# Kernel tuning notes

Hardware: AMD Instinct MI355X
Metric: run time of the kernel (lower is better)

Reference implementation:

```python
import jax, jax.numpy as jnp
import numpy as np

B, L, E, D = 32, 1024, 512, 512  # batch, seq_len, input_size, per-direction hidden
SCALE = 1.4142135623730951  # rescale=True, highway_bias=0 -> sqrt(1+exp(0*2)) = sqrt(2)


def setup_inputs() -> dict:
    key = jax.random.key(0)
    ks = jax.random.split(key, 12)
    g = lambda k, shape, s: (jax.random.normal(k, shape, jnp.float32) * s)
    return {
        "seqs": jax.random.normal(ks[0], (B, L, E), jnp.float32),
        # layer 0: input E -> 2 dirs * 4 projections * D
        "W0": g(ks[1], (E, 8 * D), (1.0 / E) ** 0.5),
        "vf0": g(ks[2], (2, D), 0.1), "vr0": g(ks[3], (2, D), 0.1),
        "bf0": jnp.zeros((2, D), jnp.float32), "br0": jnp.zeros((2, D), jnp.float32),
        # layer 1: input 2D -> 2 dirs * 4 projections * D
        "W1": g(ks[4], (2 * D, 8 * D), (1.0 / (2 * D)) ** 0.5),
        "vf1": g(ks[5], (2, D), 0.1), "vr1": g(ks[6], (2, D), 0.1),
        "bf1": jnp.zeros((2, D), jnp.float32), "br1": jnp.zeros((2, D), jnp.float32),
        "lengths": jax.random.randint(ks[7], (B,), 1, L + 1, dtype=jnp.int32),
    }


def _sru_dir(u, vf, vr, bf, br, reverse):
    # u: (L, B, 4, D) -> h: (L, B, D), c_T: (B, D)
    def step(c, u_t):
        xt, fp, rp, xp = u_t[:, 0], u_t[:, 1], u_t[:, 2], u_t[:, 3]
        f = jax.nn.sigmoid(fp + vf * c + bf)
        c_new = f * c + (1.0 - f) * xt
        r = jax.nn.sigmoid(rp + vr * c + br)
        h = r * c_new + (1.0 - r) * xp * SCALE
        return c_new, h

    c0 = jnp.zeros((u.shape[1], u.shape[-1]), u.dtype)
    cT, hs = jax.lax.scan(step, c0, u, reverse=reverse)
    return hs, cT


def _sru_layer(x, W, vf, vr, bf, br):
    # x: (L, B, n_in)
    Lx, Bx = x.shape[0], x.shape[1]
    U = (x @ W).reshape(Lx, Bx, 2, 4, -1)  # dirs, (x_tilde, f, r, x_resid)
    h_f, c_f = _sru_dir(U[:, :, 0], vf[0], vr[0], bf[0], br[0], False)
    h_b, c_b = _sru_dir(U[:, :, 1], vf[1], vr[1], bf[1], br[1], True)
    return jnp.concatenate([h_f, h_b], -1), jnp.concatenate([c_f, c_b], -1)


def reference(seqs, W0, vf0, vr0, bf0, br0, W1, vf1, vr1, bf1, br1, lengths):
    x = jnp.transpose(seqs, (1, 0, 2))  # (L, B, E)
    out0, _ = _sru_layer(x, W0, vf0, vr0, bf0, br0)
    out1, c1 = _sru_layer(out0, W1, vf1, vr1, bf1, br1)
    # module returns (h[1], output.transpose(0,1)): layer-1 final cell state, (B,L,2D) outputs
    return c1, jnp.transpose(out1, (1, 0, 2))
```

## Files before the change

### kernel.cpp

```cpp
#include <hip/hip_runtime.h>
#include <cstdint>
#include <cstddef>

#define B_   32
#define L_   1024
#define D_   512
#define M_   (B_ * L_)
#define N8D  4096
#define SCALEF 1.4142135623730951f
#define LOG2E 1.4426950408889634f

typedef unsigned short u16;
typedef __bf16 bf16x8 __attribute__((ext_vector_type(8)));
typedef unsigned short u16x8 __attribute__((ext_vector_type(8)));
typedef unsigned short u16x4 __attribute__((ext_vector_type(4)));
typedef float f32x4 __attribute__((ext_vector_type(4)));

__device__ __forceinline__ float bf2f(u16 u) {
    union { unsigned int i; float f; } v; v.i = ((unsigned int)u) << 16; return v.f;
}
__device__ __forceinline__ u16 f2bf(float x) {
    union { float f; unsigned int i; } v; v.f = x;
    unsigned int r = (v.i + 0x7fffu + ((v.i >> 16) & 1u)) >> 16;
    return (u16)r;
}
__device__ __forceinline__ float sigmoid_fast(float z) {
    return __builtin_amdgcn_rcpf(1.0f + __builtin_amdgcn_exp2f(-LOG2E * z));
}

__device__ __forceinline__ void gl2lds16(const u16* g, u16* l) {
    __builtin_amdgcn_global_load_lds(
        (const __attribute__((address_space(1))) void*)g,
        (__attribute__((address_space(3))) void*)l, 16, 0, 0);
}

#define VMW(n) asm volatile("s_waitcnt vmcnt(" #n ")" ::: "memory")

__global__ __launch_bounds__(256) void f32_to_bf16(const float* __restrict__ in,
                                                   u16* __restrict__ out) {
    size_t i = ((size_t)blockIdx.x * 256 + threadIdx.x) * 8;
    f32x4 v0 = *(const f32x4*)(in + i);
    f32x4 v1 = *(const f32x4*)(in + i + 4);
    u16x8 o;
#pragma unroll
    for (int q = 0; q < 4; ++q) { o[q] = f2bf(v0[q]); o[4 + q] = f2bf(v1[q]); }
    *(u16x8*)(out + i) = o;
}

__global__ __launch_bounds__(256) void transpose_w(const float* __restrict__ in,
                                                   u16* __restrict__ out,
                                                   int R, int C) {
    __shared__ u16 tile[32][33];
    int bx = blockIdx.x * 32;
    int by = blockIdx.y * 32;
    int tx = threadIdx.x & 31;
    int ty = threadIdx.x >> 5;
#pragma unroll
    for (int i = 0; i < 32; i += 8)
        tile[ty + i][tx] = f2bf(in[(size_t)(by + ty + i) * C + bx + tx]);
    __syncthreads();
#pragma unroll
    for (int i = 0; i < 32; i += 8) {
        int n = bx + ty + i;
        int p = (n >> 11) * 2048 + ((n & 511) << 2) + ((n >> 9) & 3);
        out[(size_t)p * R + by + tx] = tile[tx][ty + i];
    }
}

__global__ __launch_bounds__(512) void gemm256(const u16* __restrict__ A,
                                               const u16* __restrict__ BT,
                                               u16* __restrict__ U, int K) {
    extern __shared__ __align__(16) u16 lds[];
    const int t    = threadIdx.x;
    const int lane = t & 63;
    const int wave = t >> 6;
    const int wm   = wave >> 2;
    const int wn   = wave & 3;
    const int qm   = lane & 15;
    const int quad = lane >> 4;

    const int nwg = gridDim.x;
    const int wg  = blockIdx.x;
    const int swz = (wg & 7) * (nwg >> 3) + (wg >> 3);
    const int bn  = (swz & 15) << 8;
    const int bm  = (swz >> 4) << 8;

    const int P0   = t * 16;
    const int L0   = P0 ^ ((P0 >> 3) & 0x30);
    const int srow = L0 >> 6;
    const int scol = (L0 & 63) >> 1;
    const u16* Ag = A  + (size_t)(bm + srow) * K + scol;
    const u16* Bg = BT + (size_t)(bn + srow) * K + scol;
    const size_t g128 = (size_t)128 * K;
    u16* ldst = lds + t * 8;

    const int fxor  = (quad * 16) ^ ((qm & 6) << 3);
    const int aBase = (wm * 128 + qm) * 64 + fxor;
    const int bBase = (wn * 64  + qm) * 64 + fxor;
    const char* ldsc = (const char*)lds;

    f32x4 acc[8][4];
#pragma unroll
    for (int i = 0; i < 8; ++i)
#pragma unroll
        for (int j = 0; j < 4; ++j) acc[i][j] = (f32x4)(0.0f);

    bf16x8 bfr[4];

#define STG(op, tile, ks, buf) do {                                          \
        const u16* g_ = ((op) ? Bg : Ag) + (size_t)(tile) * 64 + (ks) * 32;  \
        u16* l_ = ldst + (buf) * 32768 + (op) * 16384 + (ks) * 8192;         \
        gl2lds16(g_, l_);                                                    \
        gl2lds16(g_ + g128, l_ + 4096);                                      \
    } while (0)

#define PHASE(buf, mh, ks, STAGE_STMT, VM_STMT) do {                         \
        const char* As_ = ldsc + ((buf) * 32768 + (ks) * 8192) * 2;          \
        const char* Bs_ = ldsc + ((buf) * 32768 + 16384 + (ks) * 8192) * 2;  \
        bf16x8 a_[4];                                                        \
        _Pragma("unroll")                                                    \
        for (int mi = 0; mi < 4; ++mi)                                       \
            a_[mi] = *(const bf16x8*)(As_ + aBase + ((mh) * 64 + mi * 16) * 64); \
        if ((mh) == 0) {                                                     \
            _Pragma("unroll")                                                \
            for (int nj = 0; nj < 4; ++nj)                                   \
                bfr[nj] = *(const bf16x8*)(Bs_ + bBase + nj * 16 * 64);      \
        }                                                                    \
        STAGE_STMT;                                                          \
        __builtin_amdgcn_s_barrier();                                        \
        asm volatile("s_waitcnt lgkmcnt(0)" ::: "memory");                   \
        __builtin_amdgcn_sched_barrier(0);                                   \
        __builtin_amdgcn_s_setprio(1);                                       \
        _Pragma("unroll")                                                    \
        for (int mi = 0; mi < 4; ++mi)                                       \
            _Pragma("unroll")                                                \
            for (int nj = 0; nj < 4; ++nj)                                   \
                acc[(mh) * 4 + mi][nj] = __builtin_amdgcn_mfma_f32_16x16x32_bf16( \
                    a_[mi], bfr[nj], acc[(mh) * 4 + mi][nj], 0, 0, 0);       \
        __builtin_amdgcn_s_setprio(0);                                       \
        VM_STMT;                                                             \
        __builtin_amdgcn_s_barrier();                                        \
    } while (0)

    const int nt = K >> 6;

    STG(1, 0, 0, 0); STG(0, 0, 0, 0); STG(1, 0, 1, 0); STG(0, 0, 1, 0);
    VMW(4);
    STG(1, 1, 0, 1); STG(0, 1, 0, 1); STG(1, 1, 1, 1);
    VMW(6);
    __builtin_amdgcn_s_barrier();

    const int niter = (nt >> 1) - 1;
    for (int i = 0; i < niter; ++i) {
        const int tp1 = 2 * i + 1, tp2 = 2 * i + 2, tp3 = 2 * i + 3;
        PHASE(0, 0, 0, STG(0, tp1, 1, 1), );
        PHASE(0, 1, 0, STG(1, tp2, 0, 0), );
        PHASE(0, 0, 1, STG(0, tp2, 0, 0), );
        PHASE(0, 1, 1, STG(1, tp2, 1, 0), VMW(6));
        PHASE(1, 0, 0, STG(0, tp2, 1, 0), );
        PHASE(1, 1, 0, STG(1, tp3, 0, 1), );
        PHASE(1, 0, 1, STG(0, tp3, 0, 1), );
        PHASE(1, 1, 1, STG(1, tp3, 1, 1), VMW(6));
    }
    PHASE(0, 0, 0, STG(0, nt - 1, 1, 1), );
    PHASE(0, 1, 0, , );
    PHASE(0, 0, 1, , );
    PHASE(0, 1, 1, , VMW(4));
    PHASE(1, 0, 0, , );
    PHASE(1, 1, 0, , VMW(0));
    PHASE(1, 0, 1, , );
    PHASE(1, 1, 1, , );

#undef PHASE
#undef STG

#pragma unroll
    for (int i8 = 0; i8 < 8; ++i8) {
        const int row0 = bm + wm * 128 + (i8 >> 2) * 64 + (i8 & 3) * 16 + quad * 4;
#pragma unroll
        for (int nj = 0; nj < 4; ++nj) {
            const int col = bn + wn * 64 + nj * 16 + qm;
#pragma unroll
            for (int r = 0; r < 4; ++r)
                U[(size_t)(row0 + r) * N8D + col] = f2bf(acc[i8][nj][r]);
        }
    }
}

template<bool OUT_F32>
__global__ __launch_bounds__(256) void sru_scan(const u16* __restrict__ U,
                                                const float* __restrict__ vf,
                                                const float* __restrict__ vr,
                                                const float* __restrict__ bfv,
                                                const float* __restrict__ brv,
                                                void* __restrict__ Hv,
                                                void* __restrict__ Cv) {
    constexpr int PF = 32;
    constexpr int NB = L_ / PF;

    int gid = blockIdx.x * blockDim.x + threadIdx.x;
    int d   = gid & (D_ - 1);
    int dir = (gid >> 9) & 1;
    int b   = gid >> 10;
    int ch  = dir * D_ + d;

    const float vf_v = vf[ch];
    const float vr_v = vr[ch];
    const float bf_v = bfv[ch];
    const float br_v = brv[ch];

    const ptrdiff_t ustep = dir ? -(ptrdiff_t)N8D : (ptrdiff_t)N8D;
    const ptrdiff_t hstep = dir ? -(ptrdiff_t)1024 : (ptrdiff_t)1024;
    const u16* p0 = U + (size_t)b * L_ * N8D + dir * 2048 + d * 4
                      + (dir ? (size_t)(L_ - 1) * N8D : 0);
    const size_t hstart = (size_t)b * L_ * 1024 + ch + (dir ? (size_t)(L_ - 1) * 1024 : 0);
    float* Hf = (float*)Hv + hstart;
    u16*   Hh = (u16*)Hv + hstart;

    float c = 0.0f;

    auto loadB = [&](u16x4 (&buf)[PF], int tb) {
        const u16* base = p0 + (ptrdiff_t)tb * PF * ustep;
#pragma unroll
        for (int i = 0; i < PF; ++i)
            buf[i] = *(const u16x4*)(base + (ptrdiff_t)i * ustep);
    };
    auto compStore = [&](u16x4 (&buf)[PF], int tb) {
        const ptrdiff_t hb = (ptrdiff_t)tb * PF * hstep;
#pragma unroll
        for (int i = 0; i < PF; ++i) {
            float xt = bf2f(buf[i][0]), fp = bf2f(buf[i][1]);
            float rp = bf2f(buf[i][2]), xp = bf2f(buf[i][3]);
            float f = sigmoid_fast(fp + vf_v * c + bf_v);
            float r = sigmoid_fast(rp + vr_v * c + br_v);
            c = f * (c - xt) + xt;
            float xs = xp * SCALEF;
            float h  = r * (c - xs) + xs;
            ptrdiff_t ho = hb + (ptrdiff_t)i * hstep;
            if (OUT_F32) Hf[ho] = h; else Hh[ho] = f2bf(h);
        }
    };

    u16x4 b0[PF], b1[PF];
    loadB(b0, 0);
    loadB(b1, 1);
    for (int t = 0; t < NB; t += 2) {
        compStore(b0, t);
        if (t + 2 < NB) loadB(b0, t + 2);
        compStore(b1, t + 1);
        if (t + 3 < NB) loadB(b1, t + 3);
    }

    if (OUT_F32) ((float*)Cv)[b * 1024 + ch] = c;
    else         ((u16*)Cv)[b * 1024 + ch]  = f2bf(c);
}

extern "C" void kernel_launch(void* const* d_in, const int* in_sizes, int n_in,
                              void* d_out, int out_size, void* d_ws, size_t ws_size,
                              hipStream_t stream) {
    (void)in_sizes; (void)n_in; (void)out_size; (void)ws_size;

    const float* seqs = (const float*)d_in[0];
    const float* W0   = (const float*)d_in[1];
    const float* vf0  = (const float*)d_in[2];
    const float* vr0  = (const float*)d_in[3];
    const float* bf0  = (const float*)d_in[4];
    const float* br0  = (const float*)d_in[5];
    const float* W1   = (const float*)d_in[6];
    const float* vf1  = (const float*)d_in[7];
    const float* vr1  = (const float*)d_in[8];
    const float* bf1  = (const float*)d_in[9];
    const float* br1  = (const float*)d_in[10];

    float* out = (float*)d_out;
    char* ws = (char*)d_ws;

    const size_t U_BYTES  = (size_t)M_ * N8D * 2;
    const size_t H_BYTES  = (size_t)M_ * 1024 * 2;
    const size_t W0T_B    = (size_t)4096 * 512 * 2;
    const size_t W1T_B    = (size_t)4096 * 1024 * 2;

    u16* U   = (u16*)(ws);
    u16* H0  = (u16*)(ws + U_BYTES);
    u16* S16 = H0;
    u16* W0T = (u16*)(ws + U_BYTES + H_BYTES);
    u16* W1T = (u16*)(ws + U_BYTES + H_BYTES + W0T_B);
    u16* Cd  = (u16*)(ws + U_BYTES + H_BYTES + W0T_B + W1T_B);

    f32_to_bf16<<<dim3(M_ * 512 / 8 / 256), 256, 0, stream>>>(seqs, S16);

    transpose_w<<<dim3(4096 / 32, 512 / 32), 256, 0, stream>>>(W0, W0T, 512, 4096);
    transpose_w<<<dim3(4096 / 32, 1024 / 32), 256, 0, stream>>>(W1, W1T, 1024, 4096);

    gemm256<<<dim3(2048), 512, 131072, stream>>>(S16, W0T, U, 512);
    sru_scan<false><<<dim3(M_ / 256), 256, 0, stream>>>(U, vf0, vr0, bf0, br0, (void*)H0, (void*)Cd);

    gemm256<<<dim3(2048), 512, 131072, stream>>>(H0, W1T, U, 1024);
    sru_scan<true><<<dim3(M_ / 256), 256, 0, stream>>>(U, vf1, vr1, bf1, br1,
                                                       (void*)(out + B_ * 1024), (void*)out);
}
```

Baseline: 856.0 us.

## Prefetch GEMM LDS fragments into registers and spread SRU scan across more blocks

The GEMM main loop now reads the next phase's A and B fragments from LDS into a second set of registers while the current 16 MFMAs run. This hides LDS read latency behind matrix math, and launch_bounds asks for two blocks per CU. The SRU scan keeps the same 32768 threads but launches them as 512 blocks of 64 instead of 128 blocks of 256, so the latency-bound recurrence spreads over more CUs. The extra fragment registers plus the two-block occupancy hint may force register spills in the GEMM, and one block per CU is still likely given its 128 KB of LDS.

```diff
diff --git a/kernel.cpp b/kernel.cpp
--- a/kernel.cpp
+++ b/kernel.cpp
@@ -67,9 +67,9 @@
     }
 }
 
-__global__ __launch_bounds__(512) void gemm256(const u16* __restrict__ A,
-                                               const u16* __restrict__ BT,
-                                               u16* __restrict__ U, int K) {
+__global__ __launch_bounds__(512, 2) void gemm256(const u16* __restrict__ A,
+                                                  const u16* __restrict__ BT,
+                                                  u16* __restrict__ U, int K) {
     extern __shared__ __align__(16) u16 lds[];
     const int t    = threadIdx.x;
     const int lane = t & 63;
@@ -105,7 +105,8 @@
 #pragma unroll
         for (int j = 0; j < 4; ++j) acc[i][j] = (f32x4)(0.0f);
 
-    bf16x8 bfr[4];
+    bf16x8 aA[4], aB[4];
+    bf16x8 bK0[4], bK1[4];
 
 #define STG(op, tile, ks, buf) do {                                          \
         const u16* g_ = ((op) ? Bg : Ag) + (size_t)(tile) * 64 + (ks) * 32;  \
@@ -114,19 +115,21 @@
         gl2lds16(g_ + g128, l_ + 4096);                                      \
     } while (0)
 
-#define PHASE(buf, mh, ks, STAGE_STMT, VM_STMT) do {                         \
-        const char* As_ = ldsc + ((buf) * 32768 + (ks) * 8192) * 2;          \
-        const char* Bs_ = ldsc + ((buf) * 32768 + 16384 + (ks) * 8192) * 2;  \
-        bf16x8 a_[4];                                                        \
+#define RD_A(dst, buf, ks, mh) do {                                          \
         _Pragma("unroll")                                                    \
         for (int mi = 0; mi < 4; ++mi)                                       \
-            a_[mi] = *(const bf16x8*)(As_ + aBase + ((mh) * 64 + mi * 16) * 64); \
-        if ((mh) == 0) {                                                     \
-            _Pragma("unroll")                                                \
-            for (int nj = 0; nj < 4; ++nj)                                   \
-                bfr[nj] = *(const bf16x8*)(Bs_ + bBase + nj * 16 * 64);      \
-        }                                                                    \
-        STAGE_STMT;                                                          \
+            dst[mi] = *(const bf16x8*)(ldsc + ((buf) * 65536 + (ks) * 16384) \
+                          + aBase + ((mh) * 64 + mi * 16) * 64);             \
+    } while (0)
+
+#define RD_B(dst, buf, ks) do {                                              \
+        _Pragma("unroll")                                                    \
+        for (int nj = 0; nj < 4; ++nj)                                       \
+            dst[nj] = *(const bf16x8*)(ldsc + ((buf) * 65536 + 32768 +       \
+                          (ks) * 16384) + bBase + nj * 16 * 64);             \
+    } while (0)
+
+#define MFMA16(mh, AU, BU) do {                                              \
         __builtin_amdgcn_s_barrier();                                        \
         asm volatile("s_waitcnt lgkmcnt(0)" ::: "memory");                   \
         __builtin_amdgcn_sched_barrier(0);                                   \
@@ -136,11 +139,11 @@
             _Pragma("unroll")                                                \
             for (int nj = 0; nj < 4; ++nj)                                   \
                 acc[(mh) * 4 + mi][nj] = __builtin_amdgcn_mfma_f32_16x16x32_bf16( \
-                    a_[mi], bfr[nj], acc[(mh) * 4 + mi][nj], 0, 0, 0);       \
+                    AU[mi], BU[nj], acc[(mh) * 4 + mi][nj], 0, 0, 0);        \
         __builtin_amdgcn_s_setprio(0);                                       \
-        VM_STMT;                                                             \
-        __builtin_amdgcn_s_barrier();                                        \
     } while (0)
+
+#define BARB __builtin_amdgcn_s_barrier()
 
     const int nt = K >> 6;
 
@@ -149,29 +152,33 @@
     STG(1, 1, 0, 1); STG(0, 1, 0, 1); STG(1, 1, 1, 1);
     VMW(6);
     __builtin_amdgcn_s_barrier();
+    RD_A(aA, 0, 0, 0); RD_B(bK0, 0, 0);
 
     const int niter = (nt >> 1) - 1;
     for (int i = 0; i < niter; ++i) {
         const int tp1 = 2 * i + 1, tp2 = 2 * i + 2, tp3 = 2 * i + 3;
-        PHASE(0, 0, 0, STG(0, tp1, 1, 1), );
-        PHASE(0, 1, 0, STG(1, tp2, 0, 0), );
-        PHASE(0, 0, 1, STG(0, tp2, 0, 0), );
-        PHASE(0, 1, 1, STG(1, tp2, 1, 0), VMW(6));
-        PHASE(1, 0, 0, STG(0, tp2, 1, 0), );
-        PHASE(1, 1, 0, STG(1, tp3, 0, 1), );
-        PHASE(1, 0, 1, STG(0, tp3, 0, 1), );
-        PHASE(1, 1, 1, STG(1, tp3, 1, 1), VMW(6));
+        STG(0, tp1, 1, 1); MFMA16(0, aA, bK0); RD_A(aB, 0, 0, 1); BARB;
+        STG(1, tp2, 0, 0); MFMA16(1, aB, bK0); RD_A(aA, 0, 1, 0); RD_B(bK1, 0, 1); BARB;
+        STG(0, tp2, 0, 0); MFMA16(0, aA, bK1); RD_A(aB, 0, 1, 1); BARB;
+        STG(1, tp2, 1, 0); MFMA16(1, aB, bK1); VMW(6); RD_A(aA, 1, 0, 0); RD_B(bK0, 1, 0); BARB;
+        STG(0, tp2, 1, 0); MFMA16(0, aA, bK0); RD_A(aB, 1, 0, 1); BARB;
+        STG(1, tp3, 0, 1); MFMA16(1, aB, bK0); RD_A(aA, 1, 1, 0); RD_B(bK1, 1, 1); BARB;
+        STG(0, tp3, 0, 1); MFMA16(0, aA, bK1); RD_A(aB, 1, 1, 1); BARB;
+        STG(1, tp3, 1, 1); MFMA16(1, aB, bK1); VMW(6); RD_A(aA, 0, 0, 0); RD_B(bK0, 0, 0); BARB;
     }
-    PHASE(0, 0, 0, STG(0, nt - 1, 1, 1), );
-    PHASE(0, 1, 0, , );
-    PHASE(0, 0, 1, , );
-    PHASE(0, 1, 1, , VMW(4));
-    PHASE(1, 0, 0, , );
-    PHASE(1, 1, 0, , VMW(0));
-    PHASE(1, 0, 1, , );
-    PHASE(1, 1, 1, , );
-
-#undef PHASE
+    STG(0, nt - 1, 1, 1); MFMA16(0, aA, bK0); RD_A(aB, 0, 0, 1); BARB;
+    MFMA16(1, aB, bK0); RD_A(aA, 0, 1, 0); RD_B(bK1, 0, 1); BARB;
+    MFMA16(0, aA, bK1); RD_A(aB, 0, 1, 1); BARB;
+    MFMA16(1, aB, bK1); VMW(4); RD_A(aA, 1, 0, 0); RD_B(bK0, 1, 0); BARB;
+    MFMA16(0, aA, bK0); RD_A(aB, 1, 0, 1); BARB;
+    MFMA16(1, aB, bK0); VMW(0); RD_A(aA, 1, 1, 0); RD_B(bK1, 1, 1); BARB;
+    MFMA16(0, aA, bK1); RD_A(aB, 1, 1, 1); BARB;
+    MFMA16(1, aB, bK1); BARB;
+
+#undef BARB
+#undef MFMA16
+#undef RD_B
+#undef RD_A
 #undef STG
 
 #pragma unroll
@@ -188,13 +195,13 @@
 }
 
 template<bool OUT_F32>
-__global__ __launch_bounds__(256) void sru_scan(const u16* __restrict__ U,
-                                                const float* __restrict__ vf,
-                                                const float* __restrict__ vr,
-                                                const float* __restrict__ bfv,
-                                                const float* __restrict__ brv,
-                                                void* __restrict__ Hv,
-                                                void* __restrict__ Cv) {
+__global__ __launch_bounds__(64) void sru_scan(const u16* __restrict__ U,
+                                               const float* __restrict__ vf,
+                                               const float* __restrict__ vr,
+                                               const float* __restrict__ bfv,
+                                               const float* __restrict__ brv,
+                                               void* __restrict__ Hv,
+                                               void* __restrict__ Cv) {
     constexpr int PF = 32;
     constexpr int NB = L_ / PF;
 
@@ -293,9 +300,9 @@
     transpose_w<<<dim3(4096 / 32, 1024 / 32), 256, 0, stream>>>(W1, W1T, 1024, 4096);
 
     gemm256<<<dim3(2048), 512, 131072, stream>>>(S16, W0T, U, 512);
-    sru_scan<false><<<dim3(M_ / 256), 256, 0, stream>>>(U, vf0, vr0, bf0, br0, (void*)H0, (void*)Cd);
+    sru_scan<false><<<dim3(512), 64, 0, stream>>>(U, vf0, vr0, bf0, br0, (void*)H0, (void*)Cd);
 
     gemm256<<<dim3(2048), 512, 131072, stream>>>(H0, W1T, U, 1024);
-    sru_scan<true><<<dim3(M_ / 256), 256, 0, stream>>>(U, vf1, vr1, bf1, br1,
-                                                       (void*)(out + B_ * 1024), (void*)out);
-}
+    sru_scan<true><<<dim3(512), 64, 0, stream>>>(U, vf1, vr1, bf1, br1,
+                                                 (void*)(out + B_ * 1024), (void*)out);
+}
```

New measurement: 774.5 us. 9.5% less time.
